# Kernel optimization log

Measured on AMD Instinct MI355X. Metric: run time of the kernel, lower is better.

Reference implementation:

```python
import jax, jax.numpy as jnp
import numpy as np

B, T, D, H, O = 1024, 256, 63, 128, 14


def _lstm_dir(x, W_ih, W_hh, b_ih, b_hh):
    """Single-direction LSTM over x [B,T,D] -> hidden outputs [B,T,H].
    PyTorch gate order: i, f, g, o."""
    # Precompute input projection for all timesteps (one big GEMM).
    xp = x @ W_ih.T + (b_ih + b_hh)  # [B,T,4H]

    def step(carry, xt):
        h, c = carry
        gates = xt + h @ W_hh.T  # [B,4H]
        i, f, g, o = jnp.split(gates, 4, axis=-1)
        i = jax.nn.sigmoid(i)
        f = jax.nn.sigmoid(f)
        g = jnp.tanh(g)
        o = jax.nn.sigmoid(o)
        c = f * c + i * g
        h = o * jnp.tanh(c)
        return (h, c), h

    h0 = jnp.zeros((x.shape[0], W_hh.shape[1]), x.dtype)
    (_, _), hs = jax.lax.scan(step, (h0, h0), jnp.swapaxes(xp, 0, 1))
    return jnp.swapaxes(hs, 0, 1)  # [B,T,H]


def setup_inputs() -> dict:
    key = jax.random.key(0)
    ks = jax.random.split(key, 11)
    s = 1.0 / np.sqrt(H)  # PyTorch LSTM init scale
    return {
        "x": jax.random.normal(ks[0], (B, T, D), jnp.float32),
        "W_ih_f": jax.random.uniform(ks[1], (4 * H, D), jnp.float32, -s, s),
        "W_hh_f": jax.random.uniform(ks[2], (4 * H, H), jnp.float32, -s, s),
        "b_ih_f": jax.random.uniform(ks[3], (4 * H,), jnp.float32, -s, s),
        "b_hh_f": jax.random.uniform(ks[4], (4 * H,), jnp.float32, -s, s),
        "W_ih_b": jax.random.uniform(ks[5], (4 * H, D), jnp.float32, -s, s),
        "W_hh_b": jax.random.uniform(ks[6], (4 * H, H), jnp.float32, -s, s),
        "b_ih_b": jax.random.uniform(ks[7], (4 * H,), jnp.float32, -s, s),
        "b_hh_b": jax.random.uniform(ks[8], (4 * H,), jnp.float32, -s, s),
        "W_fc": jax.random.uniform(ks[9], (O, 2 * H), jnp.float32, -s, s),
        "b_fc": jax.random.uniform(ks[10], (O,), jnp.float32, -s, s),
    }


def reference(x, W_ih_f, W_hh_f, b_ih_f, b_hh_f,
              W_ih_b, W_hh_b, b_ih_b, b_hh_b, W_fc, b_fc):
    h_f = _lstm_dir(x, W_ih_f, W_hh_f, b_ih_f, b_hh_f)            # fwd dir
    h_b = _lstm_dir(x[:, ::-1], W_ih_b, W_hh_b, b_ih_b, b_hh_b)[:, ::-1]  # bwd dir
    # out[:, -1, :] of the BiLSTM; dropout is identity at inference.
    last = jnp.concatenate([h_f[:, -1], h_b[:, -1]], axis=-1)  # [B, 2H]
    return last @ W_fc.T + b_fc  # [B, O]
```

## Files before the change

kernel.cpp:

```cpp
#include <hip/hip_runtime.h>

typedef __attribute__((ext_vector_type(8))) short bf16x8;
typedef __attribute__((ext_vector_type(4))) float f32x4;

#define BB 1024
#define TT 256
#define DD 63
#define HH 128
#define CHUNK 4
#define HSTR 160
#define XSTR2 72
#define NSTR4 520
#define CT 4

#define LDS_BARRIER() asm volatile("s_waitcnt lgkmcnt(0)\n\ts_barrier" ::: "memory")

__device__ __forceinline__ short f2bf(float f) {
  unsigned u = __builtin_bit_cast(unsigned, f);
  u = (u + 0x7FFFu + ((u >> 16) & 1u)) >> 16;
  return (short)u;
}
__device__ __forceinline__ float sigm(float x) {
  return __builtin_amdgcn_rcpf(1.f + __expf(-x));
}
__device__ __forceinline__ float tanh_fast(float x) {
  float e = __expf(2.f * x);
  return 1.f - 2.f * __builtin_amdgcn_rcpf(e + 1.f);
}

__global__ __launch_bounds__(512, 2)
void bilstm_fused_kernel(const float* __restrict__ X,
                         const float* __restrict__ Wih,
                         const float* __restrict__ Whh,
                         const float* __restrict__ bih,
                         const float* __restrict__ bhh,
                         const float* __restrict__ Wih_b,
                         const float* __restrict__ bih_b,
                         const float* __restrict__ bhh_b,
                         const float* __restrict__ Wfc,
                         const float* __restrict__ bfc,
                         float* __restrict__ out) {
  __shared__ __align__(16) short hbuf[2 * 4 * HSTR];
  __shared__ __align__(16) float xpbuf[16 * NSTR4];
  __shared__ __align__(16) short xstage[2 * 16 * XSTR2];
  __shared__ __align__(16) float fst[4 * 256];
  __shared__ __align__(16) float xl[4 * 64];
  __shared__ __align__(16) float glb[4 * 512];

  const int tid  = threadIdx.x;
  const int wave = tid >> 6;
  const int lane = tid & 63;
  const int quad = lane >> 4;
  const int l15  = lane & 15;
  const int b0   = blockIdx.x * CHUNK;
  const int br   = l15 & 3;
  const int p    = l15 >> 2;

  bf16x8 Ah[4][4];
  bf16x8 Axw[4][2];
  f32x4  bias[4];
#pragma unroll
  for (int g = 0; g < 4; ++g) {
    const int n = g * 128 + wave * 16 + l15;
    const float* wr = Whh + (size_t)n * HH;
#pragma unroll
    for (int ks = 0; ks < 4; ++ks) {
      const int k0 = ks * 32 + quad * 8;
      f32x4 w0 = *(const f32x4*)(wr + k0);
      f32x4 w1 = *(const f32x4*)(wr + k0 + 4);
      bf16x8 v;
#pragma unroll
      for (int jj = 0; jj < 4; ++jj) { v[jj] = f2bf(w0[jj]); v[4 + jj] = f2bf(w1[jj]); }
      Ah[g][ks] = v;
    }
    const float* xr = Wih + (size_t)n * DD;
#pragma unroll
    for (int ks = 0; ks < 2; ++ks) {
      const int k0 = ks * 32 + quad * 8;
      bf16x8 v;
#pragma unroll
      for (int jj = 0; jj < 8; ++jj) {
        const int k = k0 + jj;
        v[jj] = (k < DD) ? f2bf(xr[k]) : (short)0;
      }
      Axw[g][ks] = v;
    }
    const int cb = g * 128 + wave * 16 + quad * 4;
    f32x4 b1 = *(const f32x4*)&bih[cb];
    f32x4 b2 = *(const f32x4*)&bhh[cb];
    bias[g] = b1 + b2;
  }

  for (int i = tid; i < 2 * 4 * HSTR; i += 512) hbuf[i] = 0;
  if (tid < 32) {
    const int bufc = tid >> 4, c = tid & 15;
    xstage[bufc * 16 * XSTR2 + c * XSTR2 + DD] = 0;
  }

  const bool sthr = (tid < 252);
  int so_[4];
  const float* sx_[4];
#pragma unroll
  for (int j = 0; j < 4; ++j) {
    const int e = tid + 252 * j;
    const int c = e / DD, k = e - DD * c;
    so_[j] = c * XSTR2 + k;
    sx_[j] = X + ((size_t)(b0 + (c & 3)) * TT + (c >> 2)) * DD + k;
  }

  if (sthr) {
#pragma unroll
    for (int j = 0; j < 4; ++j) xstage[so_[j]] = f2bf(sx_[j][0]);
  }
  float xr1_[4];
  if (sthr) {
#pragma unroll
    for (int j = 0; j < 4; ++j) xr1_[j] = sx_[j][CT * DD];
  }
  __syncthreads();
#pragma unroll
  for (int g = 0; g < 4; ++g) {
    bf16x8 B0 = *(const bf16x8*)&xstage[l15 * XSTR2 + quad * 8];
    bf16x8 B1 = *(const bf16x8*)&xstage[l15 * XSTR2 + 32 + quad * 8];
    f32x4 px = __builtin_amdgcn_mfma_f32_16x16x32_bf16(Axw[g][0], B0, bias[g], 0, 0, 0);
    px = __builtin_amdgcn_mfma_f32_16x16x32_bf16(Axw[g][1], B1, px, 0, 0, 0);
    *(f32x4*)&xpbuf[l15 * NSTR4 + g * 128 + wave * 16 + quad * 4] = px;
  }
  if (sthr) {
#pragma unroll
    for (int j = 0; j < 4; ++j) xstage[16 * XSTR2 + so_[j]] = f2bf(xr1_[j]);
  }
  __syncthreads();

  float cc = 0.f, hv = 0.f;
  const int hcol = wave * 16 + quad * 4 + p;
  const bool s0 = (l15 & 4) != 0;
  const bool s1 = (l15 & 8) != 0;

  for (int cu = 0; cu < TT / CT; ++cu) {
    const int t0 = cu * CT;
    float xr_[4];
    f32x4 pxp[4];
#pragma unroll
    for (int s = 0; s < CT; ++s) {
      const int t = t0 + s;
      const int hcur = (t & 1) * (4 * HSTR);

      if (s == 0 && cu <= TT / CT - 3 && sthr) {
#pragma unroll
        for (int j = 0; j < 4; ++j) xr_[j] = sx_[j][(size_t)(t0 + 2 * CT) * DD];
      }

      bf16x8 Bh_[4];
#pragma unroll
      for (int ks = 0; ks < 4; ++ks)
        Bh_[ks] = *(const bf16x8*)&hbuf[hcur + br * HSTR + ks * 32 + quad * 8];

      if (cu < TT / CT - 1) {
        const int xs = ((cu + 1) & 1) * (16 * XSTR2);
        bf16x8 B0 = *(const bf16x8*)&xstage[xs + l15 * XSTR2 + quad * 8];
        bf16x8 B1 = *(const bf16x8*)&xstage[xs + l15 * XSTR2 + 32 + quad * 8];
        f32x4 px = __builtin_amdgcn_mfma_f32_16x16x32_bf16(Axw[s][0], B0, bias[s], 0, 0, 0);
        pxp[s] = __builtin_amdgcn_mfma_f32_16x16x32_bf16(Axw[s][1], B1, px, 0, 0, 0);
      }

      float gact[4];
#pragma unroll
      for (int g = 0; g < 4; ++g) {
        f32x4 ci = *(const f32x4*)&xpbuf[(s * 4 + br) * NSTR4 + g * 128 + wave * 16 + quad * 4];
        f32x4 a = __builtin_amdgcn_mfma_f32_16x16x32_bf16(Ah[g][0], Bh_[0], ci, 0, 0, 0);
        a = __builtin_amdgcn_mfma_f32_16x16x32_bf16(Ah[g][1], Bh_[1], a, 0, 0, 0);
        a = __builtin_amdgcn_mfma_f32_16x16x32_bf16(Ah[g][2], Bh_[2], a, 0, 0, 0);
        a = __builtin_amdgcn_mfma_f32_16x16x32_bf16(Ah[g][3], Bh_[3], a, 0, 0, 0);
        const float a01 = s0 ? a[1] : a[0];
        const float a23 = s0 ? a[3] : a[2];
        const float v = s1 ? a23 : a01;
        gact[g] = (g == 2) ? tanh_fast(v) : sigm(v);
      }

      cc = gact[1] * cc + gact[0] * gact[2];
      hv = gact[3] * tanh_fast(cc);
      hbuf[(hcur ^ (4 * HSTR)) + br * HSTR + hcol] = f2bf(hv);

      if (s < CT - 1 || cu == TT / CT - 1) {
        LDS_BARRIER();
      } else {
        LDS_BARRIER();
#pragma unroll
        for (int g = 0; g < 4; ++g)
          *(f32x4*)&xpbuf[l15 * NSTR4 + g * 128 + wave * 16 + quad * 4] = pxp[g];
        if (cu <= TT / CT - 3 && sthr) {
          const int xd2 = (cu & 1) * (16 * XSTR2);
#pragma unroll
          for (int j = 0; j < 4; ++j) xstage[xd2 + so_[j]] = f2bf(xr_[j]);
        }
        LDS_BARRIER();
      }
    }
  }

  fst[br * 256 + hcol] = hv;
  {
    const int xrow = tid / DD;
    const int xd   = tid - xrow * DD;
    if (tid < CHUNK * DD)
      xl[xrow * 64 + xd] = X[((size_t)(b0 + xrow) * TT + (TT - 1)) * DD + xd];
  }
  __syncthreads();

  {
    const int n = tid;
    const float* wr = Wih_b + (size_t)n * DD;
    const float bb2 = bih_b[n] + bhh_b[n];
    float a0 = bb2, a1 = bb2, a2 = bb2, a3 = bb2;
    for (int k = 0; k < DD; ++k) {
      const float w = wr[k];
      a0 += w * xl[0 * 64 + k];
      a1 += w * xl[1 * 64 + k];
      a2 += w * xl[2 * 64 + k];
      a3 += w * xl[3 * 64 + k];
    }
    glb[0 * 512 + n] = a0;
    glb[1 * 512 + n] = a1;
    glb[2 * 512 + n] = a2;
    glb[3 * 512 + n] = a3;
  }
  __syncthreads();

  {
    const int b = tid >> 7, j = tid & 127;
    const float iv = sigm(glb[b * 512 + j]);
    const float gv = tanh_fast(glb[b * 512 + 256 + j]);
    const float ov = sigm(glb[b * 512 + 384 + j]);
    fst[b * 256 + 128 + j] = ov * tanh_fast(iv * gv);
  }
  __syncthreads();

  if (tid < CHUNK * 14) {
    const int rr = tid / 14, o = tid - rr * 14;
    const float* wr = Wfc + (size_t)o * (2 * HH);
    float acc = bfc[o];
#pragma unroll 16
    for (int k = 0; k < 2 * HH; ++k) acc += wr[k] * fst[rr * 256 + k];
    out[(size_t)(b0 + rr) * 14 + o] = acc;
  }
}

extern "C" void kernel_launch(void* const* d_in, const int* in_sizes, int n_in,
                              void* d_out, int out_size, void* d_ws, size_t ws_size,
                              hipStream_t stream) {
  const float* X     = (const float*)d_in[0];
  const float* Wih_f = (const float*)d_in[1];
  const float* Whh_f = (const float*)d_in[2];
  const float* bih_f = (const float*)d_in[3];
  const float* bhh_f = (const float*)d_in[4];
  const float* Wih_b = (const float*)d_in[5];
  const float* bih_b = (const float*)d_in[7];
  const float* bhh_b = (const float*)d_in[8];
  const float* Wfc   = (const float*)d_in[9];
  const float* bfc   = (const float*)d_in[10];
  float* out = (float*)d_out;

  bilstm_fused_kernel<<<BB / CHUNK, 512, 0, stream>>>(
      X, Wih_f, Whh_f, bih_f, bhh_f, Wih_b, bih_b, bhh_b, Wfc, bfc, out);
}
```

Before: 269.4 us.

## Keep input projections in registers and redistribute via ds_bpermute instead of LDS

Removes the xpbuf LDS staging of the precomputed input-projection tiles. Results stay in registers (pcur/pnew) and are shuffled to the lanes that need them with ds_bpermute. This drops one of the two barriers at each chunk boundary and moves the next-chunk projection MFMAs after the gate computation, off the critical path. The cost is 16 bpermute ops per step, which still use LDS hardware and add latency inside the serial recurrence, plus higher register pressure.

```diff
diff --git a/kernel.cpp b/kernel.cpp
--- a/kernel.cpp
+++ b/kernel.cpp
@@ -10,7 +10,6 @@
 #define CHUNK 4
 #define HSTR 160
 #define XSTR2 72
-#define NSTR4 520
 #define CT 4
 
 #define LDS_BARRIER() asm volatile("s_waitcnt lgkmcnt(0)\n\ts_barrier" ::: "memory")
@@ -26,6 +25,10 @@
 __device__ __forceinline__ float tanh_fast(float x) {
   float e = __expf(2.f * x);
   return 1.f - 2.f * __builtin_amdgcn_rcpf(e + 1.f);
+}
+__device__ __forceinline__ float bperm_f(int addr, float v) {
+  return __builtin_bit_cast(float,
+      __builtin_amdgcn_ds_bpermute(addr, __builtin_bit_cast(int, v)));
 }
 
 __global__ __launch_bounds__(512, 2)
@@ -41,7 +44,6 @@
                          const float* __restrict__ bfc,
                          float* __restrict__ out) {
   __shared__ __align__(16) short hbuf[2 * 4 * HSTR];
-  __shared__ __align__(16) float xpbuf[16 * NSTR4];
   __shared__ __align__(16) short xstage[2 * 16 * XSTR2];
   __shared__ __align__(16) float fst[4 * 256];
   __shared__ __align__(16) float xl[4 * 64];
@@ -54,7 +56,8 @@
   const int l15  = lane & 15;
   const int b0   = blockIdx.x * CHUNK;
   const int br   = l15 & 3;
-  const int p    = l15 >> 2;
+
+  const int pbase = (((lane & 48) | (lane & 3)) << 2);
 
   bf16x8 Ah[4][4];
   bf16x8 Axw[4][2];
@@ -118,13 +121,13 @@
     for (int j = 0; j < 4; ++j) xr1_[j] = sx_[j][CT * DD];
   }
   __syncthreads();
+  f32x4 pcur[4];
 #pragma unroll
   for (int g = 0; g < 4; ++g) {
     bf16x8 B0 = *(const bf16x8*)&xstage[l15 * XSTR2 + quad * 8];
     bf16x8 B1 = *(const bf16x8*)&xstage[l15 * XSTR2 + 32 + quad * 8];
     f32x4 px = __builtin_amdgcn_mfma_f32_16x16x32_bf16(Axw[g][0], B0, bias[g], 0, 0, 0);
-    px = __builtin_amdgcn_mfma_f32_16x16x32_bf16(Axw[g][1], B1, px, 0, 0, 0);
-    *(f32x4*)&xpbuf[l15 * NSTR4 + g * 128 + wave * 16 + quad * 4] = px;
+    pcur[g] = __builtin_amdgcn_mfma_f32_16x16x32_bf16(Axw[g][1], B1, px, 0, 0, 0);
   }
   if (sthr) {
 #pragma unroll
@@ -133,22 +136,21 @@
   __syncthreads();
 
   float cc = 0.f, hv = 0.f;
-  const int hcol = wave * 16 + quad * 4 + p;
+  const int hcol = wave * 16 + quad * 4 + (l15 >> 2);
   const bool s0 = (l15 & 4) != 0;
   const bool s1 = (l15 & 8) != 0;
 
   for (int cu = 0; cu < TT / CT; ++cu) {
-    const int t0 = cu * CT;
     float xr_[4];
-    f32x4 pxp[4];
+    f32x4 pnew[4];
 #pragma unroll
     for (int s = 0; s < CT; ++s) {
-      const int t = t0 + s;
+      const int t = cu * CT + s;
       const int hcur = (t & 1) * (4 * HSTR);
 
       if (s == 0 && cu <= TT / CT - 3 && sthr) {
 #pragma unroll
-        for (int j = 0; j < 4; ++j) xr_[j] = sx_[j][(size_t)(t0 + 2 * CT) * DD];
+        for (int j = 0; j < 4; ++j) xr_[j] = sx_[j][(size_t)(cu + 2) * CT * DD];
       }
 
       bf16x8 Bh_[4];
@@ -156,18 +158,23 @@
       for (int ks = 0; ks < 4; ++ks)
         Bh_[ks] = *(const bf16x8*)&hbuf[hcur + br * HSTR + ks * 32 + quad * 8];
 
+      bf16x8 Bx0, Bx1;
       if (cu < TT / CT - 1) {
         const int xs = ((cu + 1) & 1) * (16 * XSTR2);
-        bf16x8 B0 = *(const bf16x8*)&xstage[xs + l15 * XSTR2 + quad * 8];
-        bf16x8 B1 = *(const bf16x8*)&xstage[xs + l15 * XSTR2 + 32 + quad * 8];
-        f32x4 px = __builtin_amdgcn_mfma_f32_16x16x32_bf16(Axw[s][0], B0, bias[s], 0, 0, 0);
-        pxp[s] = __builtin_amdgcn_mfma_f32_16x16x32_bf16(Axw[s][1], B1, px, 0, 0, 0);
-      }
+        Bx0 = *(const bf16x8*)&xstage[xs + l15 * XSTR2 + quad * 8];
+        Bx1 = *(const bf16x8*)&xstage[xs + l15 * XSTR2 + 32 + quad * 8];
+      }
+
+      const int paddr = pbase + (s << 4);
 
       float gact[4];
 #pragma unroll
       for (int g = 0; g < 4; ++g) {
-        f32x4 ci = *(const f32x4*)&xpbuf[(s * 4 + br) * NSTR4 + g * 128 + wave * 16 + quad * 4];
+        f32x4 ci;
+        ci[0] = bperm_f(paddr, pcur[g][0]);
+        ci[1] = bperm_f(paddr, pcur[g][1]);
+        ci[2] = bperm_f(paddr, pcur[g][2]);
+        ci[3] = bperm_f(paddr, pcur[g][3]);
         f32x4 a = __builtin_amdgcn_mfma_f32_16x16x32_bf16(Ah[g][0], Bh_[0], ci, 0, 0, 0);
         a = __builtin_amdgcn_mfma_f32_16x16x32_bf16(Ah[g][1], Bh_[1], a, 0, 0, 0);
         a = __builtin_amdgcn_mfma_f32_16x16x32_bf16(Ah[g][2], Bh_[2], a, 0, 0, 0);
@@ -178,24 +185,27 @@
         gact[g] = (g == 2) ? tanh_fast(v) : sigm(v);
       }
 
+      if (cu < TT / CT - 1) {
+        f32x4 px = __builtin_amdgcn_mfma_f32_16x16x32_bf16(Axw[s][0], Bx0, bias[s], 0, 0, 0);
+        pnew[s] = __builtin_amdgcn_mfma_f32_16x16x32_bf16(Axw[s][1], Bx1, px, 0, 0, 0);
+      }
+
       cc = gact[1] * cc + gact[0] * gact[2];
       hv = gact[3] * tanh_fast(cc);
       hbuf[(hcur ^ (4 * HSTR)) + br * HSTR + hcol] = f2bf(hv);
 
-      if (s < CT - 1 || cu == TT / CT - 1) {
-        LDS_BARRIER();
-      } else {
-        LDS_BARRIER();
-#pragma unroll
-        for (int g = 0; g < 4; ++g)
-          *(f32x4*)&xpbuf[l15 * NSTR4 + g * 128 + wave * 16 + quad * 4] = pxp[g];
+      if (s == CT - 1) {
         if (cu <= TT / CT - 3 && sthr) {
           const int xd2 = (cu & 1) * (16 * XSTR2);
 #pragma unroll
           for (int j = 0; j < 4; ++j) xstage[xd2 + so_[j]] = f2bf(xr_[j]);
         }
-        LDS_BARRIER();
-      }
+        if (cu < TT / CT - 1) {
+          pcur[0] = pnew[0]; pcur[1] = pnew[1];
+          pcur[2] = pnew[2]; pcur[3] = pnew[3];
+        }
+      }
+      LDS_BARRIER();
     }
   }
 
```

Measured after the change: 295.0 us. +9.5%, slower.
